# Optimization experiments

Hardware: AMD Instinct MI355X
Metric: run time of the kernel (lower is better)

Reference implementation:

```python
import jax, jax.numpy as jnp
import numpy as np

ROUTINGS = 3
EPS = 1e-05


def squash(x, axis):
    n = jnp.linalg.norm(x, axis=axis, keepdims=True)
    n2 = n * n
    return n2 / (1.0 + n2) * x / (n + EPS)


def setup_inputs() -> dict:
    key = jax.random.key(0)
    k1, k2, k3 = jax.random.split(key, 3)
    B, I, O = 64, 1024, 1024
    stdv = 1.0 / np.sqrt(I)
    u = jax.random.normal(k1, (B, I), dtype=jnp.float32)
    weight = jax.random.uniform(k2, (I, O), dtype=jnp.float32, minval=-stdv, maxval=stdv)
    bias = jax.random.uniform(k3, (O,), dtype=jnp.float32, minval=-stdv, maxval=stdv)
    return {"u": u, "weight": weight, "bias": bias}


def reference(u, weight, bias):
    # u: [B, I], weight: [I, O], bias: [O]
    O = weight.shape[1]
    u_hat = u[:, :, None] * weight  # [B, I, O]
    # retain_grad=False: routing iterations use detached u_hat / bias
    uh = jax.lax.stop_gradient(u_hat)
    bs = jax.lax.stop_gradient(bias)
    c = jnp.full((1, 1, O), 1.0 / O, dtype=u.dtype)  # softmax(zeros) over out dim
    b = jnp.zeros_like(uh)
    for _ in range(ROUTINGS - 1):
        v = squash(jnp.sum(uh * c, axis=1) + bs, axis=1)  # [B, O]
        b = b + uh * v[:, None, :]
        c = jax.nn.softmax(b, axis=2)
    return squash(jnp.sum(u_hat * c, axis=1) + bias, axis=1)
```

## Files before the change

kernel.cpp:

```cpp
#include <hip/hip_runtime.h>
#include <math.h>


#define BB 64
#define II 1024
#define OO 1024
#define EPSF 1e-5f
#define LOG2E 1.44269504088896340736f

__device__ __forceinline__ float wave_sum(float v) {
    #pragma unroll
    for (int off = 32; off > 0; off >>= 1)
        v += __shfl_xor(v, off, 64);
    return v;
}
__device__ __forceinline__ float rfl(float x) {
    return __int_as_float(__builtin_amdgcn_readfirstlane(__float_as_int(x)));
}

template<int IBLKS>
__global__ __launch_bounds__(256)
__attribute__((amdgpu_waves_per_eu(4, 4)))
void stage_k(
    const float* __restrict__ u, const float* __restrict__ w,
    const float* __restrict__ v, float* __restrict__ part)
{
    constexpr int IPB = II / IBLKS;
    constexpr int NG  = IPB / 8;
    static_assert(IPB % 8 == 0, "need groups of 8");
    const int bg   = blockIdx.x / IBLKS;
    const int iblk = blockIdx.x % IBLKS;
    const int wave = threadIdx.x >> 6;
    const int lane = threadIdx.x & 63;
    const int b    = bg * 4 + wave;
    const float4* w4 = (const float4*)w;
    const float4* v4 = (const float4*)(v + b * OO);

    float vv[16];
    #pragma unroll
    for (int j = 0; j < 4; j++) {
        float4 a = v4[j * 64 + lane];
        vv[j*4+0]=a.x*LOG2E; vv[j*4+1]=a.y*LOG2E;
        vv[j*4+2]=a.z*LOG2E; vv[j*4+3]=a.w*LOG2E;
    }
    float ar[16];
    #pragma unroll
    for (int k = 0; k < 16; k++) ar[k] = 0.f;

    const int i0 = iblk * IPB;
    #pragma unroll 1
    for (int g = 0; g < NG; g++) {
        const int ib = i0 + g * 8;

        float us[8];
        #pragma unroll
        for (int ii = 0; ii < 8; ii++)
            us[ii] = rfl(u[b * II + ib + ii]);

        float sA[8];
        #pragma unroll 2
        for (int ii = 0; ii < 8; ii++) {
            const int i = ib + ii;
            float a0;
            {
                float4 t = w4[i * 256 + 0 * 64 + lane];
                a0 = __builtin_amdgcn_exp2f((t.x * vv[0]) * us[ii])
                   + __builtin_amdgcn_exp2f((t.y * vv[1]) * us[ii])
                   + __builtin_amdgcn_exp2f((t.z * vv[2]) * us[ii])
                   + __builtin_amdgcn_exp2f((t.w * vv[3]) * us[ii]);
            }
            #pragma unroll
            for (int j = 1; j < 4; j++) {
                float4 t = w4[i * 256 + j * 64 + lane];
                a0 += __builtin_amdgcn_exp2f((t.x * vv[j*4+0]) * us[ii])
                    + __builtin_amdgcn_exp2f((t.y * vv[j*4+1]) * us[ii])
                    + __builtin_amdgcn_exp2f((t.z * vv[j*4+2]) * us[ii])
                    + __builtin_amdgcn_exp2f((t.w * vv[j*4+3]) * us[ii]);
            }
            sA[ii] = a0;
        }
        #pragma unroll
        for (int off = 32; off > 0; off >>= 1) {
            #pragma unroll
            for (int ii = 0; ii < 8; ii++)
                sA[ii] += __shfl_xor(sA[ii], off, 64);
        }
        float qs[8];
        #pragma unroll
        for (int ii = 0; ii < 8; ii++)
            qs[ii] = rfl(us[ii] * __builtin_amdgcn_rcpf(sA[ii]));

        #pragma unroll 2
        for (int ii = 0; ii < 8; ii++) {
            const int i = ib + ii;
            #pragma unroll
            for (int j = 0; j < 4; j++) {
                float4 t = w4[i * 256 + j * 64 + lane];
                float p;
                p = __builtin_amdgcn_exp2f((t.x * vv[j*4+0]) * us[ii]);
                ar[j*4+0] = fmaf(t.x * p, qs[ii], ar[j*4+0]);
                p = __builtin_amdgcn_exp2f((t.y * vv[j*4+1]) * us[ii]);
                ar[j*4+1] = fmaf(t.y * p, qs[ii], ar[j*4+1]);
                p = __builtin_amdgcn_exp2f((t.z * vv[j*4+2]) * us[ii]);
                ar[j*4+2] = fmaf(t.z * p, qs[ii], ar[j*4+2]);
                p = __builtin_amdgcn_exp2f((t.w * vv[j*4+3]) * us[ii]);
                ar[j*4+3] = fmaf(t.w * p, qs[ii], ar[j*4+3]);
            }
        }
    }
    float4* dst = (float4*)(part + ((size_t)iblk * BB + b) * OO);
    #pragma unroll
    for (int j = 0; j < 4; j++) {
        float4 o;
        o.x = ar[j*4+0]; o.y = ar[j*4+1]; o.z = ar[j*4+2]; o.w = ar[j*4+3];
        dst[j * 64 + lane] = o;
    }
}

template<int IBLKS>
__global__ __launch_bounds__(256)
__attribute__((amdgpu_waves_per_eu(4, 4)))
void gemm_k(
    const float* __restrict__ u, const float* __restrict__ w,
    float* __restrict__ part)
{
    constexpr int IPB = II / IBLKS;
    const int bg   = blockIdx.x / IBLKS;
    const int iblk = blockIdx.x % IBLKS;
    const int wave = threadIdx.x >> 6;
    const int lane = threadIdx.x & 63;
    const int b    = bg * 4 + wave;
    const float4* w4 = (const float4*)w;

    float ar[16];
    #pragma unroll
    for (int k = 0; k < 16; k++) ar[k] = 0.f;

    const int i0 = iblk * IPB;
    #pragma unroll 2
    for (int ii = 0; ii < IPB; ii++) {
        const int i = i0 + ii;
        const float ub = rfl(u[b * II + i]);
        #pragma unroll
        for (int j = 0; j < 4; j++) {
            float4 t = w4[i * 256 + j * 64 + lane];
            ar[j*4+0] = fmaf(ub, t.x, ar[j*4+0]);
            ar[j*4+1] = fmaf(ub, t.y, ar[j*4+1]);
            ar[j*4+2] = fmaf(ub, t.z, ar[j*4+2]);
            ar[j*4+3] = fmaf(ub, t.w, ar[j*4+3]);
        }
    }
    float4* dst = (float4*)(part + ((size_t)iblk * BB + b) * OO);
    #pragma unroll
    for (int j = 0; j < 4; j++) {
        float4 o;
        o.x = ar[j*4+0]; o.y = ar[j*4+1]; o.z = ar[j*4+2]; o.w = ar[j*4+3];
        dst[j * 64 + lane] = o;
    }
}

__global__ __launch_bounds__(1024) void reduce_squash(
    const float* __restrict__ part, const float* __restrict__ bias,
    float* __restrict__ vbuf, float* __restrict__ out,
    float scale, int mode, int nblk)
{
    const int b  = blockIdx.x;
    const int t  = threadIdx.x;
    const int qd = t & 255;
    const int sl = t >> 8;
    const int per = nblk >> 2;
    const float4* p4 = (const float4*)part;

    float4 a0 = make_float4(0.f, 0.f, 0.f, 0.f), a1 = a0;
    const int k0 = sl * per;
    #pragma unroll 2
    for (int k = 0; k < per; k += 2) {
        float4 p0 = p4[(size_t)((k0 + k)     * BB + b) * 256 + qd];
        float4 p1 = p4[(size_t)((k0 + k + 1) * BB + b) * 256 + qd];
        a0.x += p0.x; a0.y += p0.y; a0.z += p0.z; a0.w += p0.w;
        a1.x += p1.x; a1.y += p1.y; a1.z += p1.z; a1.w += p1.w;
    }
    a0.x += a1.x; a0.y += a1.y; a0.z += a1.z; a0.w += a1.w;

    __shared__ float4 redq[1024];
    redq[t] = a0;
    __syncthreads();

    float ss = 0.f;
    float4 x;
    if (t < 256) {
        float4 r0 = redq[qd], r1 = redq[256 + qd],
               r2 = redq[512 + qd], r3 = redq[768 + qd];
        float4 s;
        s.x = (r0.x + r1.x) + (r2.x + r3.x);
        s.y = (r0.y + r1.y) + (r2.y + r3.y);
        s.z = (r0.z + r1.z) + (r2.z + r3.z);
        s.w = (r0.w + r1.w) + (r2.w + r3.w);
        float4 bb = ((const float4*)bias)[qd];
        x.x = fmaf(s.x, scale, bb.x); x.y = fmaf(s.y, scale, bb.y);
        x.z = fmaf(s.z, scale, bb.z); x.w = fmaf(s.w, scale, bb.w);
        ss = x.x*x.x + x.y*x.y + x.z*x.z + x.w*x.w;
    }
    ss = wave_sum(ss);
    __shared__ float red2[16];
    if ((t & 63) == 0) red2[t >> 6] = ss;
    __syncthreads();
    const float tot = (red2[0] + red2[1]) + (red2[2] + red2[3]);

    if (t < 256) {
        const float n = sqrtf(tot);
        const float f = tot / ((1.f + tot) * (n + EPSF));
        float4 vo;
        vo.x = x.x * f; vo.y = x.y * f; vo.z = x.z * f; vo.w = x.w * f;
        if (mode == 0) {
            ((float4*)(vbuf + b * OO))[qd] = vo;
        } else if (mode == 1) {
            float4 pv = ((const float4*)(vbuf + b * OO))[qd];
            pv.x += vo.x; pv.y += vo.y; pv.z += vo.z; pv.w += vo.w;
            ((float4*)(vbuf + b * OO))[qd] = pv;
        } else {
            ((float4*)(out + b * OO))[qd] = vo;
        }
    }
}

template<int IBLKS>
static void run_pipeline(const float* u, const float* w, const float* bias,
                         float* out, void* d_ws, hipStream_t stream)
{
    float* part = (float*)d_ws;
    float* vbuf = part + (size_t)IBLKS * BB * OO;
    dim3 g((BB / 4) * IBLKS), blk(256), rblk(1024);
    gemm_k<IBLKS><<<g, blk, 0, stream>>>(u, w, part);
    reduce_squash<<<dim3(BB), rblk, 0, stream>>>(part, bias, vbuf, out,
                                                 1.0f / (float)OO, 0, IBLKS);
    stage_k<IBLKS><<<g, blk, 0, stream>>>(u, w, vbuf, part);
    reduce_squash<<<dim3(BB), rblk, 0, stream>>>(part, bias, vbuf, out,
                                                 1.0f, 1, IBLKS);
    stage_k<IBLKS><<<g, blk, 0, stream>>>(u, w, vbuf, part);
    reduce_squash<<<dim3(BB), rblk, 0, stream>>>(part, bias, vbuf, out,
                                                 1.0f, 2, IBLKS);
}

extern "C" void kernel_launch(void* const* d_in, const int* in_sizes, int n_in,
                              void* d_out, int out_size, void* d_ws, size_t ws_size,
                              hipStream_t stream) {
    (void)in_sizes; (void)n_in; (void)out_size;
    const float* u    = (const float*)d_in[0];
    const float* w    = (const float*)d_in[1];
    const float* bias = (const float*)d_in[2];
    float* out = (float*)d_out;

    const size_t row = (size_t)BB * OO * sizeof(float);
    if      (ws_size >= 65 * row) run_pipeline<64>(u, w, bias, out, d_ws, stream);
    else if (ws_size >= 33 * row) run_pipeline<32>(u, w, bias, out, d_ws, stream);
    else if (ws_size >= 17 * row) run_pipeline<16>(u, w, bias, out, d_ws, stream);
    else                          run_pipeline<8>(u, w, bias, out, d_ws, stream);
}
```

Baseline: 148.7 us.

## Split output dimension across wave pairs with shared-memory softmax denominator exchange

Each batch row is now handled by two waves, each covering half of the output columns, so the grid doubles and per-wave register state halves. In the routing stage, the partial softmax denominators from the two halves are exchanged through double-buffered shared memory with a block barrier each group. The fixed waves-per-EU attribute is dropped and the gemm loop unroll is increased. This raises parallelism and occupancy at the cost of a barrier per 8-row group and less reuse of each u load across output columns.

```diff
diff --git a/kernel.cpp b/kernel.cpp
--- a/kernel.cpp
+++ b/kernel.cpp
@@ -19,9 +19,7 @@
 }
 
 template<int IBLKS>
-__global__ __launch_bounds__(256)
-__attribute__((amdgpu_waves_per_eu(4, 4)))
-void stage_k(
+__global__ __launch_bounds__(256) void stage_k(
     const float* __restrict__ u, const float* __restrict__ w,
     const float* __restrict__ v, float* __restrict__ part)
 {
@@ -32,20 +30,23 @@
     const int iblk = blockIdx.x % IBLKS;
     const int wave = threadIdx.x >> 6;
     const int lane = threadIdx.x & 63;
-    const int b    = bg * 4 + wave;
+    const int b    = bg * 2 + (wave >> 1);
+    const int oh   = wave & 1;
     const float4* w4 = (const float4*)w;
     const float4* v4 = (const float4*)(v + b * OO);
 
-    float vv[16];
-    #pragma unroll
-    for (int j = 0; j < 4; j++) {
-        float4 a = v4[j * 64 + lane];
+    __shared__ float ex[2][4][8];
+
+    float vv[8];
+    #pragma unroll
+    for (int j = 0; j < 2; j++) {
+        float4 a = v4[oh * 128 + j * 64 + lane];
         vv[j*4+0]=a.x*LOG2E; vv[j*4+1]=a.y*LOG2E;
         vv[j*4+2]=a.z*LOG2E; vv[j*4+3]=a.w*LOG2E;
     }
-    float ar[16];
-    #pragma unroll
-    for (int k = 0; k < 16; k++) ar[k] = 0.f;
+    float ar[8];
+    #pragma unroll
+    for (int k = 0; k < 8; k++) ar[k] = 0.f;
 
     const int i0 = iblk * IPB;
     #pragma unroll 1
@@ -61,17 +62,10 @@
         #pragma unroll 2
         for (int ii = 0; ii < 8; ii++) {
             const int i = ib + ii;
-            float a0;
-            {
-                float4 t = w4[i * 256 + 0 * 64 + lane];
-                a0 = __builtin_amdgcn_exp2f((t.x * vv[0]) * us[ii])
-                   + __builtin_amdgcn_exp2f((t.y * vv[1]) * us[ii])
-                   + __builtin_amdgcn_exp2f((t.z * vv[2]) * us[ii])
-                   + __builtin_amdgcn_exp2f((t.w * vv[3]) * us[ii]);
-            }
-            #pragma unroll
-            for (int j = 1; j < 4; j++) {
-                float4 t = w4[i * 256 + j * 64 + lane];
+            float a0 = 0.f;
+            #pragma unroll
+            for (int j = 0; j < 2; j++) {
+                float4 t = w4[i * 256 + oh * 128 + j * 64 + lane];
                 a0 += __builtin_amdgcn_exp2f((t.x * vv[j*4+0]) * us[ii])
                     + __builtin_amdgcn_exp2f((t.y * vv[j*4+1]) * us[ii])
                     + __builtin_amdgcn_exp2f((t.z * vv[j*4+2]) * us[ii])
@@ -85,17 +79,25 @@
             for (int ii = 0; ii < 8; ii++)
                 sA[ii] += __shfl_xor(sA[ii], off, 64);
         }
+        if (lane == 0) {
+            #pragma unroll
+            for (int ii = 0; ii < 8; ii++)
+                ex[g & 1][wave][ii] = sA[ii];
+        }
+        __syncthreads();
         float qs[8];
         #pragma unroll
-        for (int ii = 0; ii < 8; ii++)
-            qs[ii] = rfl(us[ii] * __builtin_amdgcn_rcpf(sA[ii]));
+        for (int ii = 0; ii < 8; ii++) {
+            const float d = sA[ii] + ex[g & 1][wave ^ 1][ii];
+            qs[ii] = rfl(us[ii] * __builtin_amdgcn_rcpf(d));
+        }
 
         #pragma unroll 2
         for (int ii = 0; ii < 8; ii++) {
             const int i = ib + ii;
             #pragma unroll
-            for (int j = 0; j < 4; j++) {
-                float4 t = w4[i * 256 + j * 64 + lane];
+            for (int j = 0; j < 2; j++) {
+                float4 t = w4[i * 256 + oh * 128 + j * 64 + lane];
                 float p;
                 p = __builtin_amdgcn_exp2f((t.x * vv[j*4+0]) * us[ii]);
                 ar[j*4+0] = fmaf(t.x * p, qs[ii], ar[j*4+0]);
@@ -110,17 +112,15 @@
     }
     float4* dst = (float4*)(part + ((size_t)iblk * BB + b) * OO);
     #pragma unroll
-    for (int j = 0; j < 4; j++) {
+    for (int j = 0; j < 2; j++) {
         float4 o;
         o.x = ar[j*4+0]; o.y = ar[j*4+1]; o.z = ar[j*4+2]; o.w = ar[j*4+3];
-        dst[j * 64 + lane] = o;
+        dst[oh * 128 + j * 64 + lane] = o;
     }
 }
 
 template<int IBLKS>
-__global__ __launch_bounds__(256)
-__attribute__((amdgpu_waves_per_eu(4, 4)))
-void gemm_k(
+__global__ __launch_bounds__(256) void gemm_k(
     const float* __restrict__ u, const float* __restrict__ w,
     float* __restrict__ part)
 {
@@ -129,21 +129,22 @@
     const int iblk = blockIdx.x % IBLKS;
     const int wave = threadIdx.x >> 6;
     const int lane = threadIdx.x & 63;
-    const int b    = bg * 4 + wave;
+    const int b    = bg * 2 + (wave >> 1);
+    const int oh   = wave & 1;
     const float4* w4 = (const float4*)w;
 
-    float ar[16];
-    #pragma unroll
-    for (int k = 0; k < 16; k++) ar[k] = 0.f;
+    float ar[8];
+    #pragma unroll
+    for (int k = 0; k < 8; k++) ar[k] = 0.f;
 
     const int i0 = iblk * IPB;
-    #pragma unroll 2
+    #pragma unroll 4
     for (int ii = 0; ii < IPB; ii++) {
         const int i = i0 + ii;
         const float ub = rfl(u[b * II + i]);
         #pragma unroll
-        for (int j = 0; j < 4; j++) {
-            float4 t = w4[i * 256 + j * 64 + lane];
+        for (int j = 0; j < 2; j++) {
+            float4 t = w4[i * 256 + oh * 128 + j * 64 + lane];
             ar[j*4+0] = fmaf(ub, t.x, ar[j*4+0]);
             ar[j*4+1] = fmaf(ub, t.y, ar[j*4+1]);
             ar[j*4+2] = fmaf(ub, t.z, ar[j*4+2]);
@@ -152,10 +153,10 @@
     }
     float4* dst = (float4*)(part + ((size_t)iblk * BB + b) * OO);
     #pragma unroll
-    for (int j = 0; j < 4; j++) {
+    for (int j = 0; j < 2; j++) {
         float4 o;
         o.x = ar[j*4+0]; o.y = ar[j*4+1]; o.z = ar[j*4+2]; o.w = ar[j*4+3];
-        dst[j * 64 + lane] = o;
+        dst[oh * 128 + j * 64 + lane] = o;
     }
 }
 
@@ -230,7 +231,7 @@
 {
     float* part = (float*)d_ws;
     float* vbuf = part + (size_t)IBLKS * BB * OO;
-    dim3 g((BB / 4) * IBLKS), blk(256), rblk(1024);
+    dim3 g((BB / 2) * IBLKS), blk(256), rblk(1024);
     gemm_k<IBLKS><<<g, blk, 0, stream>>>(u, w, part);
     reduce_squash<<<dim3(BB), rblk, 0, stream>>>(part, bias, vbuf, out,
                                                  1.0f / (float)OO, 0, IBLKS);
```

Result: slower. 158.0 us (+6.3%).
